# Kernel optimization log

Hardware: AMD Instinct MI355X
Metric: run time of the kernel (lower is better)

Reference implementation:

```python
import jax, jax.numpy as jnp
import numpy as np

DT = 0.1
LN_EPS = 1e-5
B, T, D_IN, H, N_APP = 128, 2048, 16, 256, 10


def layer_norm(x, g, b):
    mu = jnp.mean(x, axis=-1, keepdims=True)
    var = jnp.mean(jnp.square(x - mu), axis=-1, keepdims=True)
    return (x - mu) * jax.lax.rsqrt(var + LN_EPS) * g + b


def setup_inputs() -> dict:
    key = jax.random.key(0)
    ks = jax.random.split(key, 4)
    x = jax.random.normal(ks[0], (B, T, D_IN), dtype=jnp.float32)
    W_in = jax.random.normal(ks[1], (H, D_IN), dtype=jnp.float32) * (1.0 / np.sqrt(D_IN))
    b_in = jnp.zeros((H,), dtype=jnp.float32)
    tau_param = jnp.ones((H,), dtype=jnp.float32)
    # xavier_uniform for (H, H)
    limit = np.sqrt(6.0 / (H + H))
    W_rec = jax.random.uniform(ks[2], (H, H), dtype=jnp.float32, minval=-limit, maxval=limit)
    g_intra = jnp.ones((H,), dtype=jnp.float32)
    b_intra = jnp.zeros((H,), dtype=jnp.float32)
    g_norm = jnp.ones((H,), dtype=jnp.float32)
    b_norm = jnp.zeros((H,), dtype=jnp.float32)
    W_head = jax.random.normal(ks[3], (H, N_APP), dtype=jnp.float32) * (1.0 / np.sqrt(H))
    b_head = jnp.zeros((N_APP,), dtype=jnp.float32)
    return dict(x=x, W_in=W_in, b_in=b_in, tau_param=tau_param, W_rec=W_rec,
                g_intra=g_intra, b_intra=b_intra, g_norm=g_norm, b_norm=b_norm,
                W_head=W_head, b_head=b_head)


def reference(x, W_in, b_in, tau_param, W_rec, g_intra, b_intra, g_norm, b_norm, W_head, b_head):
    # x: (B, T, D_IN)
    tau = jax.nn.softplus(tau_param)  # (H,), fixed
    # Precompute input projection for all timesteps: (B, T, H)
    inp_proj = jnp.einsum('bti,hi->bth', x, W_in) + b_in
    xs = jnp.swapaxes(inp_proj, 0, 1)  # (T, B, H) for scan

    def step(h, u_t):
        rec = h @ W_rec                       # (B, H)
        f_t = jnp.tanh(layer_norm(u_t + rec, g_intra, b_intra))
        dh = (-h / tau + f_t) * DT
        h_new = jnp.clip(h + dh, -10.0, 10.0)
        return h_new, None

    h0 = jnp.zeros((x.shape[0], W_rec.shape[0]), dtype=x.dtype)
    h, _ = jax.lax.scan(step, h0, xs)
    h = layer_norm(h, g_norm, b_norm)
    return h @ W_head + b_head  # (B, N_APP)
```

## Files before the change

### kernel.cpp

```cpp
#include <hip/hip_runtime.h>


#define BB     128
#define TT     2048
#define DIN    16
#define HH     256
#define NAPP   10
#define NT     1024
#define DT_STEP 0.1f
#define LN_EPS_C 1e-5f

typedef _Float16 half2_t __attribute__((ext_vector_type(2)));

template<int CTRL>
__device__ __forceinline__ float dpp_mov0(float x) {
    return __builtin_bit_cast(float,
        __builtin_amdgcn_update_dpp(0, __builtin_bit_cast(int, x), CTRL, 0xF, 0xF, true));
}

__device__ __forceinline__ void wave_reduce2(float& s1, float& s2) {
    s1 += dpp_mov0<0x111>(s1); s2 += dpp_mov0<0x111>(s2);
    s1 += dpp_mov0<0x112>(s1); s2 += dpp_mov0<0x112>(s2);
    s1 += dpp_mov0<0x114>(s1); s2 += dpp_mov0<0x114>(s2);
    s1 += dpp_mov0<0x118>(s1); s2 += dpp_mov0<0x118>(s2);
    s1 += dpp_mov0<0x142>(s1); s2 += dpp_mov0<0x142>(s2);
    s1 += dpp_mov0<0x143>(s1); s2 += dpp_mov0<0x143>(s2);
}

__device__ __forceinline__ half2_t as_h2(int v) { return __builtin_bit_cast(half2_t, v); }

__global__ __launch_bounds__(NT, 1)
void liquid_scan_kernel(const float* __restrict__ x,
                        const float* __restrict__ W_in,
                        const float* __restrict__ b_in,
                        const float* __restrict__ tau_param,
                        const float* __restrict__ W_rec,
                        const float* __restrict__ g_intra,
                        const float* __restrict__ b_intra,
                        const float* __restrict__ g_norm,
                        const float* __restrict__ b_norm,
                        const float* __restrict__ W_head,
                        const float* __restrict__ b_head,
                        float* __restrict__ out)
{
    const int tid  = threadIdx.x;
    const int b    = blockIdx.x;
    const int j    = tid & (HH - 1);
    const int s    = tid >> 8;
    const int wv   = tid >> 6;
    const int lane = tid & 63;

    __shared__ float part[4][HH];
    __shared__ __align__(16) float wred[4][2];
    __shared__ __align__(16) float xbuf[2][DIN];
    __shared__ unsigned int hpk_lds[HH / 2];

    half2_t w2[32];
    #pragma unroll
    for (int p = 0; p < 32; ++p) {
        const float wa = W_rec[(size_t)(s * 64 + 2 * p)     * HH + j];
        const float wb = W_rec[(size_t)(s * 64 + 2 * p + 1) * HH + j];
        half2_t t2; t2.x = (_Float16)wa; t2.y = (_Float16)wb;
        w2[p] = t2;
    }

    float win[DIN];
    float bi = 0.f;
    if (s == 1) {
        bi = b_in[j];
        #pragma unroll
        for (int k = 0; k < DIN; ++k) win[k] = W_in[j * DIN + k];
    }
    float gi = 0.f, bbi = 0.f, gn = 0.f, bn = 0.f, itau = 0.f;
    if (s == 0) {
        gi = g_intra[j]; bbi = b_intra[j]; gn = g_norm[j]; bn = b_norm[j];
        const float tp  = tau_param[j];
        const float tau = (tp > 20.f) ? tp : log1pf(__expf(tp));
        itau = 1.f / tau;
    }

    float hj = 0.f;
    if (tid < HH / 2) hpk_lds[tid] = 0u;
    const size_t xbase = (size_t)b * TT * DIN;
    if (tid < DIN) xbuf[0][tid] = x[xbase + tid];
    __syncthreads();

    const int pl = tid - (NT - DIN);

    for (int t = 0; t < TT; ++t) {
        float xv = 0.f;
        if (pl >= 0 && t + 1 < TT)
            xv = x[xbase + (size_t)(t + 1) * DIN + pl];

        const int hpk = (int)hpk_lds[(s << 5) + (lane & 31)];

        float a0 = 0.f, a1 = 0.f, a2 = 0.f, a3 = 0.f;
        #pragma unroll
        for (int p = 0; p < 32; p += 4) {
            const int r0 = __builtin_amdgcn_readlane(hpk, p + 0);
            const int r1 = __builtin_amdgcn_readlane(hpk, p + 1);
            const int r2 = __builtin_amdgcn_readlane(hpk, p + 2);
            const int r3 = __builtin_amdgcn_readlane(hpk, p + 3);
            a0 = __builtin_amdgcn_fdot2(as_h2(r0), w2[p + 0], a0, false);
            a1 = __builtin_amdgcn_fdot2(as_h2(r1), w2[p + 1], a1, false);
            a2 = __builtin_amdgcn_fdot2(as_h2(r2), w2[p + 2], a2, false);
            a3 = __builtin_amdgcn_fdot2(as_h2(r3), w2[p + 3], a3, false);
        }
        float acc = (a0 + a1) + (a2 + a3);

        if (s == 1) {
            float uin = bi;
            const float4* xb = (const float4*)xbuf[t & 1];
            const float4 x0 = xb[0], x1 = xb[1], x2 = xb[2], x3 = xb[3];
            uin = fmaf(x0.x, win[0],  uin); uin = fmaf(x0.y, win[1],  uin);
            uin = fmaf(x0.z, win[2],  uin); uin = fmaf(x0.w, win[3],  uin);
            uin = fmaf(x1.x, win[4],  uin); uin = fmaf(x1.y, win[5],  uin);
            uin = fmaf(x1.z, win[6],  uin); uin = fmaf(x1.w, win[7],  uin);
            uin = fmaf(x2.x, win[8],  uin); uin = fmaf(x2.y, win[9],  uin);
            uin = fmaf(x2.z, win[10], uin); uin = fmaf(x2.w, win[11], uin);
            uin = fmaf(x3.x, win[12], uin); uin = fmaf(x3.y, win[13], uin);
            uin = fmaf(x3.z, win[14], uin); uin = fmaf(x3.w, win[15], uin);
            part[1][j] = acc + uin;
        } else if (s >= 2) {
            part[s][j] = acc;
        }
        __syncthreads();

        float u_carry = 0.f;
        if (tid < HH) {
            const float u = acc + (part[1][j] + part[2][j]) + part[3][j];
            u_carry = u;
            float s1 = u, s2 = u * u;
            wave_reduce2(s1, s2);
            if (lane == 63) { wred[wv][0] = s1; wred[wv][1] = s2; }
        }
        __syncthreads();

        if (tid < HH) {
            const float4 ra = ((const float4*)wred)[0];
            const float4 rb = ((const float4*)wred)[1];
            const float S1 = (ra.x + ra.z) + (rb.x + rb.z);
            const float S2 = (ra.y + ra.w) + (rb.y + rb.w);
            const float mu  = S1 * (1.f / HH);
            const float var = S2 * (1.f / HH) - mu * mu;
            const float rs  = rsqrtf(var + LN_EPS_C);
            const float xn  = (u_carry - mu) * rs * gi + bbi;
            const float e = __expf(2.f * xn);
            const float f = 1.f - 2.f / (e + 1.f);
            float hn = hj + (f - hj * itau) * DT_STEP;
            hn = fminf(10.f, fmaxf(-10.f, hn));
            hj = hn;
            const float hnb = __builtin_bit_cast(float,
                __builtin_amdgcn_update_dpp(0, __builtin_bit_cast(int, hn), 0x101, 0xF, 0xF, true));
            if (!(lane & 1))
                hpk_lds[j >> 1] = __builtin_bit_cast(unsigned int,
                                   __builtin_amdgcn_cvt_pkrtz(hn, hnb));
        } else if (pl >= 0 && t + 1 < TT) {
            xbuf[(t + 1) & 1][pl] = xv;
        }
        __syncthreads();
    }

    if (tid < HH) {
        float s1 = hj, s2 = hj * hj;
        wave_reduce2(s1, s2);
        if (lane == 63) { wred[wv][0] = s1; wred[wv][1] = s2; }
    }
    __syncthreads();
    if (tid < HH) {
        const float4 ra = ((const float4*)wred)[0];
        const float4 rb = ((const float4*)wred)[1];
        const float S1 = (ra.x + ra.z) + (rb.x + rb.z);
        const float S2 = (ra.y + ra.w) + (rb.y + rb.w);
        const float mu  = S1 * (1.f / HH);
        const float var = S2 * (1.f / HH) - mu * mu;
        const float rs  = rsqrtf(var + LN_EPS_C);
        part[0][j] = (hj - mu) * rs * gn + bn;
    }
    __syncthreads();
    if (tid < NAPP) {
        float o = b_head[tid];
        for (int jj = 0; jj < HH; ++jj)
            o = fmaf(part[0][jj], W_head[jj * NAPP + tid], o);
        out[(size_t)b * NAPP + tid] = o;
    }
}

extern "C" void kernel_launch(void* const* d_in, const int* in_sizes, int n_in,
                              void* d_out, int out_size, void* d_ws, size_t ws_size,
                              hipStream_t stream) {
    const float* x       = (const float*)d_in[0];
    const float* W_in    = (const float*)d_in[1];
    const float* b_in    = (const float*)d_in[2];
    const float* tau     = (const float*)d_in[3];
    const float* W_rec   = (const float*)d_in[4];
    const float* g_intra = (const float*)d_in[5];
    const float* b_intra = (const float*)d_in[6];
    const float* g_norm  = (const float*)d_in[7];
    const float* b_norm  = (const float*)d_in[8];
    const float* W_head  = (const float*)d_in[9];
    const float* b_head  = (const float*)d_in[10];
    float* out = (float*)d_out;

    hipLaunchKernelGGL(liquid_scan_kernel, dim3(BB), dim3(NT), 0, stream,
                       x, W_in, b_in, tau, W_rec, g_intra, b_intra,
                       g_norm, b_norm, W_head, b_head, out);
}
```

Before: 1.962 ms.

## Shrink block to 256 threads, four columns per lane, single-wave LayerNorm

```diff
diff --git a/kernel.cpp b/kernel.cpp
--- a/kernel.cpp
+++ b/kernel.cpp
@@ -6,7 +6,7 @@
 #define DIN    16
 #define HH     256
 #define NAPP   10
-#define NT     1024
+#define NT     256
 #define DT_STEP 0.1f
 #define LN_EPS_C 1e-5f
 
@@ -28,6 +28,13 @@
 }
 
 __device__ __forceinline__ half2_t as_h2(int v) { return __builtin_bit_cast(half2_t, v); }
+__device__ __forceinline__ float rl63(float v) {
+    return __builtin_bit_cast(float,
+        __builtin_amdgcn_readlane(__builtin_bit_cast(int, v), 63));
+}
+__device__ __forceinline__ float softplus_f(float v) {
+    return (v > 20.f) ? v : log1pf(__expf(v));
+}
 
 __global__ __launch_bounds__(NT, 1)
 void liquid_scan_kernel(const float* __restrict__ x,
@@ -45,137 +52,135 @@
 {
     const int tid  = threadIdx.x;
     const int b    = blockIdx.x;
-    const int j    = tid & (HH - 1);
-    const int s    = tid >> 8;
-    const int wv   = tid >> 6;
     const int lane = tid & 63;
-
-    __shared__ float part[4][HH];
-    __shared__ __align__(16) float wred[4][2];
-    __shared__ __align__(16) float xbuf[2][DIN];
-    __shared__ unsigned int hpk_lds[HH / 2];
-
-    half2_t w2[32];
+    const int kq   = tid >> 6;
+    const int j0   = lane * 4;
+
+    __shared__ __align__(16) float        x_lds[TT * DIN];
+    __shared__ __align__(16) float        part[4][HH];
+    __shared__ __align__(16) unsigned int hpk_lds[HH / 2];
+
+    {
+        const float4* xg = (const float4*)(x + (size_t)b * TT * DIN);
+        float4* xl = (float4*)x_lds;
+        #pragma unroll 4
+        for (int i = tid; i < TT * DIN / 4; i += NT) xl[i] = xg[i];
+    }
+    if (tid < HH / 2) hpk_lds[tid] = 0u;
+
+    half2_t w2[4][32];
     #pragma unroll
     for (int p = 0; p < 32; ++p) {
-        const float wa = W_rec[(size_t)(s * 64 + 2 * p)     * HH + j];
-        const float wb = W_rec[(size_t)(s * 64 + 2 * p + 1) * HH + j];
-        half2_t t2; t2.x = (_Float16)wa; t2.y = (_Float16)wb;
-        w2[p] = t2;
-    }
-
-    float win[DIN];
-    float bi = 0.f;
-    if (s == 1) {
-        bi = b_in[j];
+        const float* r0 = W_rec + (size_t)(64 * kq + 2 * p) * HH + j0;
+        const float* r1 = r0 + HH;
         #pragma unroll
-        for (int k = 0; k < DIN; ++k) win[k] = W_in[j * DIN + k];
-    }
-    float gi = 0.f, bbi = 0.f, gn = 0.f, bn = 0.f, itau = 0.f;
-    if (s == 0) {
-        gi = g_intra[j]; bbi = b_intra[j]; gn = g_norm[j]; bn = b_norm[j];
-        const float tp  = tau_param[j];
-        const float tau = (tp > 20.f) ? tp : log1pf(__expf(tp));
-        itau = 1.f / tau;
-    }
-
-    float hj = 0.f;
-    if (tid < HH / 2) hpk_lds[tid] = 0u;
-    const size_t xbase = (size_t)b * TT * DIN;
-    if (tid < DIN) xbuf[0][tid] = x[xbase + tid];
+        for (int c = 0; c < 4; ++c) {
+            half2_t t2; t2.x = (_Float16)r0[c]; t2.y = (_Float16)r1[c];
+            w2[c][p] = t2;
+        }
+    }
+
+    float win[4][4];
+    #pragma unroll
+    for (int c = 0; c < 4; ++c) {
+        #pragma unroll
+        for (int r = 0; r < 4; ++r)
+            win[c][r] = W_in[(size_t)(j0 + c) * DIN + 4 * kq + r];
+    }
+
+    float bi_[4], gi_[4], bbi_[4], itau_[4], gn_[4], bn_[4];
+    float hj[4] = {0.f, 0.f, 0.f, 0.f};
+    if (kq == 0) {
+        const float4 v0 = *(const float4*)(b_in      + j0);
+        const float4 v1 = *(const float4*)(g_intra   + j0);
+        const float4 v2 = *(const float4*)(b_intra   + j0);
+        const float4 v3 = *(const float4*)(tau_param + j0);
+        const float4 v4 = *(const float4*)(g_norm    + j0);
+        const float4 v5 = *(const float4*)(b_norm    + j0);
+        bi_[0] = v0.x; bi_[1] = v0.y; bi_[2] = v0.z; bi_[3] = v0.w;
+        gi_[0] = v1.x; gi_[1] = v1.y; gi_[2] = v1.z; gi_[3] = v1.w;
+        bbi_[0] = v2.x; bbi_[1] = v2.y; bbi_[2] = v2.z; bbi_[3] = v2.w;
+        itau_[0] = 1.f / softplus_f(v3.x); itau_[1] = 1.f / softplus_f(v3.y);
+        itau_[2] = 1.f / softplus_f(v3.z); itau_[3] = 1.f / softplus_f(v3.w);
+        gn_[0] = v4.x; gn_[1] = v4.y; gn_[2] = v4.z; gn_[3] = v4.w;
+        bn_[0] = v5.x; bn_[1] = v5.y; bn_[2] = v5.z; bn_[3] = v5.w;
+    }
     __syncthreads();
 
-    const int pl = tid - (NT - DIN);
-
     for (int t = 0; t < TT; ++t) {
-        float xv = 0.f;
-        if (pl >= 0 && t + 1 < TT)
-            xv = x[xbase + (size_t)(t + 1) * DIN + pl];
-
-        const int hpk = (int)hpk_lds[(s << 5) + (lane & 31)];
+        const float4 xs = *(const float4*)&x_lds[t * DIN + 4 * kq];
+        const int hpk = (int)hpk_lds[kq * 32 + (lane & 31)];
 
         float a0 = 0.f, a1 = 0.f, a2 = 0.f, a3 = 0.f;
         #pragma unroll
-        for (int p = 0; p < 32; p += 4) {
-            const int r0 = __builtin_amdgcn_readlane(hpk, p + 0);
-            const int r1 = __builtin_amdgcn_readlane(hpk, p + 1);
-            const int r2 = __builtin_amdgcn_readlane(hpk, p + 2);
-            const int r3 = __builtin_amdgcn_readlane(hpk, p + 3);
-            a0 = __builtin_amdgcn_fdot2(as_h2(r0), w2[p + 0], a0, false);
-            a1 = __builtin_amdgcn_fdot2(as_h2(r1), w2[p + 1], a1, false);
-            a2 = __builtin_amdgcn_fdot2(as_h2(r2), w2[p + 2], a2, false);
-            a3 = __builtin_amdgcn_fdot2(as_h2(r3), w2[p + 3], a3, false);
+        for (int p = 0; p < 32; ++p) {
+            const int r = __builtin_amdgcn_readlane(hpk, p);
+            a0 = __builtin_amdgcn_fdot2(as_h2(r), w2[0][p], a0, false);
+            a1 = __builtin_amdgcn_fdot2(as_h2(r), w2[1][p], a1, false);
+            a2 = __builtin_amdgcn_fdot2(as_h2(r), w2[2][p], a2, false);
+            a3 = __builtin_amdgcn_fdot2(as_h2(r), w2[3][p], a3, false);
         }
-        float acc = (a0 + a1) + (a2 + a3);
-
-        if (s == 1) {
-            float uin = bi;
-            const float4* xb = (const float4*)xbuf[t & 1];
-            const float4 x0 = xb[0], x1 = xb[1], x2 = xb[2], x3 = xb[3];
-            uin = fmaf(x0.x, win[0],  uin); uin = fmaf(x0.y, win[1],  uin);
-            uin = fmaf(x0.z, win[2],  uin); uin = fmaf(x0.w, win[3],  uin);
-            uin = fmaf(x1.x, win[4],  uin); uin = fmaf(x1.y, win[5],  uin);
-            uin = fmaf(x1.z, win[6],  uin); uin = fmaf(x1.w, win[7],  uin);
-            uin = fmaf(x2.x, win[8],  uin); uin = fmaf(x2.y, win[9],  uin);
-            uin = fmaf(x2.z, win[10], uin); uin = fmaf(x2.w, win[11], uin);
-            uin = fmaf(x3.x, win[12], uin); uin = fmaf(x3.y, win[13], uin);
-            uin = fmaf(x3.z, win[14], uin); uin = fmaf(x3.w, win[15], uin);
-            part[1][j] = acc + uin;
-        } else if (s >= 2) {
-            part[s][j] = acc;
-        }
+        a0 = fmaf(xs.x, win[0][0], a0); a0 = fmaf(xs.y, win[0][1], a0);
+        a0 = fmaf(xs.z, win[0][2], a0); a0 = fmaf(xs.w, win[0][3], a0);
+        a1 = fmaf(xs.x, win[1][0], a1); a1 = fmaf(xs.y, win[1][1], a1);
+        a1 = fmaf(xs.z, win[1][2], a1); a1 = fmaf(xs.w, win[1][3], a1);
+        a2 = fmaf(xs.x, win[2][0], a2); a2 = fmaf(xs.y, win[2][1], a2);
+        a2 = fmaf(xs.z, win[2][2], a2); a2 = fmaf(xs.w, win[2][3], a2);
+        a3 = fmaf(xs.x, win[3][0], a3); a3 = fmaf(xs.y, win[3][1], a3);
+        a3 = fmaf(xs.z, win[3][2], a3); a3 = fmaf(xs.w, win[3][3], a3);
+
+        if (kq) ((float4*)part[kq])[lane] = make_float4(a0, a1, a2, a3);
         __syncthreads();
 
-        float u_carry = 0.f;
-        if (tid < HH) {
-            const float u = acc + (part[1][j] + part[2][j]) + part[3][j];
-            u_carry = u;
-            float s1 = u, s2 = u * u;
+        if (kq == 0) {
+            const float4 p1 = ((const float4*)part[1])[lane];
+            const float4 p2 = ((const float4*)part[2])[lane];
+            const float4 p3 = ((const float4*)part[3])[lane];
+            float u[4];
+            u[0] = a0 + (p1.x + p2.x) + (p3.x + bi_[0]);
+            u[1] = a1 + (p1.y + p2.y) + (p3.y + bi_[1]);
+            u[2] = a2 + (p1.z + p2.z) + (p3.z + bi_[2]);
+            u[3] = a3 + (p1.w + p2.w) + (p3.w + bi_[3]);
+            float s1 = (u[0] + u[1]) + (u[2] + u[3]);
+            float s2 = (u[0] * u[0] + u[1] * u[1]) + (u[2] * u[2] + u[3] * u[3]);
             wave_reduce2(s1, s2);
-            if (lane == 63) { wred[wv][0] = s1; wred[wv][1] = s2; }
-        }
-        __syncthreads();
-
-        if (tid < HH) {
-            const float4 ra = ((const float4*)wred)[0];
-            const float4 rb = ((const float4*)wred)[1];
-            const float S1 = (ra.x + ra.z) + (rb.x + rb.z);
-            const float S2 = (ra.y + ra.w) + (rb.y + rb.w);
+            const float S1 = rl63(s1);
+            const float S2 = rl63(s2);
             const float mu  = S1 * (1.f / HH);
             const float var = S2 * (1.f / HH) - mu * mu;
             const float rs  = rsqrtf(var + LN_EPS_C);
-            const float xn  = (u_carry - mu) * rs * gi + bbi;
-            const float e = __expf(2.f * xn);
-            const float f = 1.f - 2.f / (e + 1.f);
-            float hn = hj + (f - hj * itau) * DT_STEP;
-            hn = fminf(10.f, fmaxf(-10.f, hn));
-            hj = hn;
-            const float hnb = __builtin_bit_cast(float,
-                __builtin_amdgcn_update_dpp(0, __builtin_bit_cast(int, hn), 0x101, 0xF, 0xF, true));
-            if (!(lane & 1))
-                hpk_lds[j >> 1] = __builtin_bit_cast(unsigned int,
-                                   __builtin_amdgcn_cvt_pkrtz(hn, hnb));
-        } else if (pl >= 0 && t + 1 < TT) {
-            xbuf[(t + 1) & 1][pl] = xv;
+            #pragma unroll
+            for (int c = 0; c < 4; ++c) {
+                const float xn = (u[c] - mu) * rs * gi_[c] + bbi_[c];
+                const float e = __expf(2.f * xn);
+                const float f = 1.f - 2.f / (e + 1.f);
+                float v = hj[c] + (f - hj[c] * itau_[c]) * DT_STEP;
+                v = fminf(10.f, fmaxf(-10.f, v));
+                hj[c] = v;
+            }
+            uint2 pk;
+            pk.x = __builtin_bit_cast(unsigned int, __builtin_amdgcn_cvt_pkrtz(hj[0], hj[1]));
+            pk.y = __builtin_bit_cast(unsigned int, __builtin_amdgcn_cvt_pkrtz(hj[2], hj[3]));
+            ((uint2*)hpk_lds)[lane] = pk;
         }
         __syncthreads();
     }
 
-    if (tid < HH) {
-        float s1 = hj, s2 = hj * hj;
+    if (kq == 0) {
+        float s1 = (hj[0] + hj[1]) + (hj[2] + hj[3]);
+        float s2 = (hj[0] * hj[0] + hj[1] * hj[1]) + (hj[2] * hj[2] + hj[3] * hj[3]);
         wave_reduce2(s1, s2);
-        if (lane == 63) { wred[wv][0] = s1; wred[wv][1] = s2; }
-    }
-    __syncthreads();
-    if (tid < HH) {
-        const float4 ra = ((const float4*)wred)[0];
-        const float4 rb = ((const float4*)wred)[1];
-        const float S1 = (ra.x + ra.z) + (rb.x + rb.z);
-        const float S2 = (ra.y + ra.w) + (rb.y + rb.w);
+        const float S1 = rl63(s1);
+        const float S2 = rl63(s2);
         const float mu  = S1 * (1.f / HH);
         const float var = S2 * (1.f / HH) - mu * mu;
         const float rs  = rsqrtf(var + LN_EPS_C);
-        part[0][j] = (hj - mu) * rs * gn + bn;
+        float4 ho;
+        ho.x = (hj[0] - mu) * rs * gn_[0] + bn_[0];
+        ho.y = (hj[1] - mu) * rs * gn_[1] + bn_[1];
+        ho.z = (hj[2] - mu) * rs * gn_[2] + bn_[2];
+        ho.w = (hj[3] - mu) * rs * gn_[3] + bn_[3];
+        ((float4*)part[0])[lane] = ho;
     }
     __syncthreads();
     if (tid < NAPP) {
```

New measurement: 1.711 ms. 12.8% less time.
